# Kernel tuning notes

Measured on AMD Instinct MI355X. Metric: run time of the kernel, lower is better.

The kernel has to match this reference:

```python
import jax, jax.numpy as jnp
import numpy as np

KERNEL = 3
DILATIONS = (2, 3)
NUM_HEADS = 8


def _unfold_windows(t, k, dil):
    # t: [B, C, H, W] -> [B, C, k*k, H, W], same layout as nn.Unfold(k, dil, pad=dil*(k-1)//2)
    B, C, H, W = t.shape
    pad = dil * (k - 1) // 2
    tp = jnp.pad(t, ((0, 0), (0, 0), (pad, pad), (pad, pad)))
    ws = [tp[:, :, i * dil:i * dil + H, j * dil:j * dil + W]
          for i in range(k) for j in range(k)]
    return jnp.stack(ws, axis=2)


def _dilate_attention(q, k_, v, kernel, dil, head_dim):
    # q,k_,v: [B, d, H, W]
    B, d, H, W = q.shape
    nh = d // head_dim
    scale = head_dim ** (-0.5)
    qh = q.reshape(B, nh, head_dim, H, W)
    kw = _unfold_windows(k_, kernel, dil).reshape(B, nh, head_dim, kernel * kernel, H, W)
    vw = _unfold_windows(v, kernel, dil).reshape(B, nh, head_dim, kernel * kernel, H, W)
    attn = jax.nn.softmax(jnp.einsum('bndhw,bndkhw->bnkhw', qh, kw) * scale, axis=2)
    out = jnp.einsum('bnkhw,bndkhw->bndhw', attn, vw)  # [B, nh, hd, H, W]
    return out.transpose(0, 3, 4, 1, 2).reshape(B, H, W, d)


def setup_inputs() -> dict:
    key = jax.random.key(0)
    k1, k2, k3, k4 = jax.random.split(key, 4)
    B, H, W, C = 4, 128, 128, 256
    x = jax.random.normal(k1, (B, H, W, C), dtype=jnp.float32)
    Wqkv = jax.random.normal(k2, (3 * C, C), dtype=jnp.float32) * (C ** -0.5)
    Wproj = jax.random.normal(k3, (C, C), dtype=jnp.float32) * (C ** -0.5)
    bproj = jnp.zeros((C,), dtype=jnp.float32)
    return {"x": x, "Wqkv": Wqkv, "Wproj": Wproj, "bproj": bproj}


def reference(x, Wqkv, Wproj, bproj):
    B, H, W, C = x.shape
    nd = len(DILATIONS)
    head_dim = C // NUM_HEADS
    # 1x1 conv qkv (no bias), then split into 3 and nd dilation groups
    qkv = jnp.einsum('bhwc,oc->bohw', x, Wqkv).reshape(B, 3, nd, C // nd, H, W)
    outs = []
    for i, dil in enumerate(DILATIONS):
        q, k_, v = qkv[:, 0, i], qkv[:, 1, i], qkv[:, 2, i]
        outs.append(_dilate_attention(q, k_, v, KERNEL, dil, head_dim))
    xo = jnp.concatenate(outs, axis=-1)  # [B, H, W, C], dilation-group-major channels
    return jnp.einsum('bhwc,oc->bhwo', xo, Wproj) + bproj
```

## Files before the change

### kernel.cpp

```cpp
#include <hip/hip_runtime.h>
#include <stdint.h>


typedef __attribute__((ext_vector_type(8))) short bf16x8;
typedef __attribute__((ext_vector_type(4))) float f32x4;

__device__ __forceinline__ void unpack2(unsigned u, float& lo, float& hi) {
  union { unsigned u; float f; } a, b;
  a.u = u << 16;
  b.u = u & 0xffff0000u;
  lo = a.f; hi = b.f;
}
__device__ __forceinline__ unsigned short f2bf(float f) {
  union { float f; unsigned u; } x; x.f = f;
  unsigned r = x.u + 0x7fffu + ((x.u >> 16) & 1u);
  return (unsigned short)(r >> 16);
}
__device__ __forceinline__ unsigned pk2bf(float a, float b) {
  return (unsigned)f2bf(a) | ((unsigned)f2bf(b) << 16);
}

__global__ __launch_bounds__(256) void cvt_f32_to_bf16(
    const float* __restrict__ src, unsigned short* __restrict__ dst, int n) {
  int i = (blockIdx.x * 256 + threadIdx.x) * 8;
  if (i + 8 <= n) {
    const float4* s = (const float4*)(src + i);
    float4 a = s[0], b = s[1];
    uint4 o;
    o.x = pk2bf(a.x, a.y); o.y = pk2bf(a.z, a.w);
    o.z = pk2bf(b.x, b.y); o.w = pk2bf(b.z, b.w);
    *(uint4*)(dst + i) = o;
  } else {
    for (; i < n; ++i) dst[i] = f2bf(src[i]);
  }
}

#define BARX()                                                \
  do {                                                        \
    asm volatile("s_waitcnt lgkmcnt(0)" ::: "memory");        \
    __builtin_amdgcn_s_barrier();                             \
    __builtin_amdgcn_sched_barrier(0);                        \
  } while (0)
#define WAITVM(n)                                             \
  do {                                                        \
    asm volatile("s_waitcnt vmcnt(" #n ")" ::: "memory");     \
    __builtin_amdgcn_sched_barrier(0);                        \
  } while (0)

template <int OUTF32>
__global__ __launch_bounds__(256) void gemm_bt(
    const unsigned short* __restrict__ A, const unsigned short* __restrict__ B,
    void* __restrict__ Cout, const float* __restrict__ bias,
    int N, int NT) {
  __shared__ __align__(16) unsigned short lds[4][8192];

  const int tid  = threadIdx.x;
  const int lane = tid & 63;
  const int wv   = tid >> 6;
  const int wr   = wv >> 1;
  const int wc   = wv & 1;

  const int nwg = gridDim.x;
  const int q8  = nwg >> 3;
  const int nid = (blockIdx.x & 7) * q8 + (blockIdx.x >> 3);
  const int n0  = (nid % NT) * 128;
  const int m0  = (nid / NT) * 128;

  const int stg_row = wv * 8 + (lane >> 3);
  const int stg_k   = ((lane & 7) ^ (lane >> 3)) * 8;
  const unsigned short* Ag = A + (size_t)(m0 + stg_row) * 256 + stg_k;
  const unsigned short* Bg = B + (size_t)(n0 + stg_row) * 256 + stg_k;

  f32x4 acc[4][4];
#pragma unroll
  for (int i = 0; i < 4; ++i)
#pragma unroll
    for (int j = 0; j < 4; ++j) acc[i][j] = (f32x4){0.f, 0.f, 0.f, 0.f};

  const int a_r = lane & 15;
  const int rsw = lane & 7;

#define STAGE(buf, kt)                                                         \
  do {                                                                         \
    const unsigned short* Asrc = Ag + (kt) * 64;                               \
    const unsigned short* Bsrc = Bg + (kt) * 64;                               \
    _Pragma("unroll")                                                          \
    for (int it = 0; it < 4; ++it) {                                           \
      __builtin_amdgcn_global_load_lds(                                        \
          (const __attribute__((address_space(1))) void*)(Asrc + (size_t)it * 32 * 256), \
          (__attribute__((address_space(3))) void*)&lds[(buf) * 2][it * 2048 + wv * 512], \
          16, 0, 0);                                                           \
      __builtin_amdgcn_global_load_lds(                                        \
          (const __attribute__((address_space(1))) void*)(Bsrc + (size_t)it * 32 * 256), \
          (__attribute__((address_space(3))) void*)&lds[(buf) * 2 + 1][it * 2048 + wv * 512], \
          16, 0, 0);                                                           \
    }                                                                          \
  } while (0)

#define COMPUTE(buf)                                                           \
  do {                                                                         \
    _Pragma("unroll")                                                          \
    for (int kk = 0; kk < 64; kk += 32) {                                      \
      const int gsw = (((kk >> 3) + (lane >> 4)) ^ rsw) * 8;  \
      bf16x8 af[4], bfr[4];                                                    \
      _Pragma("unroll")                                                        \
      for (int mi = 0; mi < 4; ++mi)                                           \
        af[mi] = *(const bf16x8*)&lds[(buf) * 2][(wr * 64 + mi * 16 + a_r) * 64 + gsw]; \
      _Pragma("unroll")                                                        \
      for (int ni = 0; ni < 4; ++ni)                                           \
        bfr[ni] = *(const bf16x8*)&lds[(buf) * 2 + 1][(wc * 64 + ni * 16 + a_r) * 64 + gsw]; \
      _Pragma("unroll")                                                        \
      for (int mi = 0; mi < 4; ++mi)                                           \
        _Pragma("unroll")                                                      \
        for (int ni = 0; ni < 4; ++ni)                                         \
          acc[mi][ni] = __builtin_amdgcn_mfma_f32_16x16x32_bf16(               \
              af[mi], bfr[ni], acc[mi][ni], 0, 0, 0);                          \
    }                                                                          \
  } while (0)

  STAGE(0, 0);
  STAGE(1, 1);
  WAITVM(8);  BARX();
  COMPUTE(0);
  BARX();
  STAGE(0, 2);
  WAITVM(8);  BARX();
  COMPUTE(1);
  BARX();
  STAGE(1, 3);
  WAITVM(8);  BARX();
  COMPUTE(0);
  BARX();
  WAITVM(0);  BARX();
  COMPUTE(1);
  BARX();

  const int cl = wc * 64 + a_r;
  const int rl = wr * 64 + (lane >> 4) * 4;
  if (!OUTF32) {
    unsigned short* eb = &lds[0][0];
#pragma unroll
    for (int ni = 0; ni < 4; ++ni)
#pragma unroll
      for (int mi = 0; mi < 4; ++mi)
#pragma unroll
        for (int r = 0; r < 4; ++r)
          eb[(rl + mi * 16 + r) * 136 + cl + ni * 16] = f2bf(acc[mi][ni][r]);
    BARX();
    unsigned short* C = (unsigned short*)Cout;
#pragma unroll
    for (int p = 0; p < 8; ++p) {
      const int idx = p * 256 + tid;
      const int row = idx >> 4;
      const int seg = idx & 15;
      uint4 v = *(const uint4*)&eb[row * 136 + seg * 8];
      *(uint4*)&C[(size_t)(m0 + row) * N + n0 + seg * 8] = v;
    }
  } else {
    float* ef = (float*)&lds[0][0];
    float* C = (float*)Cout;
    float bv[4];
#pragma unroll
    for (int ni = 0; ni < 4; ++ni) bv[ni] = bias[n0 + wc * 64 + ni * 16 + a_r];
#pragma unroll
    for (int half = 0; half < 2; ++half) {
      if (wr == half) {
        const int rb = (lane >> 4) * 4;
#pragma unroll
        for (int ni = 0; ni < 4; ++ni)
#pragma unroll
          for (int mi = 0; mi < 4; ++mi)
#pragma unroll
            for (int r = 0; r < 4; ++r)
              ef[(rb + mi * 16 + r) * 132 + wc * 64 + ni * 16 + a_r] =
                  acc[mi][ni][r] + bv[ni];
      }
      BARX();
#pragma unroll
      for (int p = 0; p < 8; ++p) {
        const int idx = p * 256 + tid;
        const int row = idx >> 5;
        const int seg = idx & 31;
        f32x4 v = *(const f32x4*)&ef[row * 132 + seg * 4];
        *(f32x4*)&C[(size_t)(m0 + half * 64 + row) * N + n0 + seg * 4] = v;
      }
      BARX();
    }
  }
#undef STAGE
#undef COMPUTE
}

__global__ __launch_bounds__(256) void attn_kernel(
    const unsigned short* __restrict__ qkv, unsigned short* __restrict__ xo) {
  const int nwg = gridDim.x;
  const int q8  = nwg >> 3;
  const int bid = (blockIdx.x & 7) * q8 + (blockIdx.x >> 3);
  const int gid   = bid * 256 + threadIdx.x;
  const int combo = gid & 7;
  const int pixel = gid >> 3;
  const int w = pixel & 127;
  const int h = (pixel >> 7) & 127;
  const int b = pixel >> 14;
  const int branch = combo >> 2;
  const int dil = branch ? 3 : 2;
  const int choff = combo * 32;

  const unsigned short* qp = qkv + (size_t)pixel * 768 + choff;
  float q[32];
#pragma unroll
  for (int t = 0; t < 4; ++t) {
    uint4 u = *(const uint4*)(qp + t * 8);
    unpack2(u.x, q[t * 8 + 0], q[t * 8 + 1]);
    unpack2(u.y, q[t * 8 + 2], q[t * 8 + 3]);
    unpack2(u.z, q[t * 8 + 4], q[t * 8 + 5]);
    unpack2(u.w, q[t * 8 + 6], q[t * 8 + 7]);
  }

  float sc[9];
#pragma unroll
  for (int i = 0; i < 3; ++i) {
#pragma unroll
    for (int j = 0; j < 3; ++j) {
      const int hh = h + (i - 1) * dil;
      const int ww = w + (j - 1) * dil;
      float s = 0.f;
      if ((unsigned)hh < 128u && (unsigned)ww < 128u) {
        const unsigned short* kp =
            qkv + (size_t)((((b << 7) | hh) << 7) | ww) * 768 + 256 + choff;
#pragma unroll
        for (int t = 0; t < 4; ++t) {
          uint4 u = *(const uint4*)(kp + t * 8);
          float a0, a1;
          unpack2(u.x, a0, a1); s += q[t * 8 + 0] * a0 + q[t * 8 + 1] * a1;
          unpack2(u.y, a0, a1); s += q[t * 8 + 2] * a0 + q[t * 8 + 3] * a1;
          unpack2(u.z, a0, a1); s += q[t * 8 + 4] * a0 + q[t * 8 + 5] * a1;
          unpack2(u.w, a0, a1); s += q[t * 8 + 6] * a0 + q[t * 8 + 7] * a1;
        }
      }
      sc[i * 3 + j] = s * 0.17677669529663687f;
    }
  }

  float mx = sc[0];
#pragma unroll
  for (int t = 1; t < 9; ++t) mx = fmaxf(mx, sc[t]);
  float wgt[9], sum = 0.f;
#pragma unroll
  for (int t = 0; t < 9; ++t) { wgt[t] = __expf(sc[t] - mx); sum += wgt[t]; }
  const float inv = 1.f / sum;

  float o[32];
#pragma unroll
  for (int t = 0; t < 32; ++t) o[t] = 0.f;
#pragma unroll
  for (int i = 0; i < 3; ++i) {
#pragma unroll
    for (int j = 0; j < 3; ++j) {
      const int hh = h + (i - 1) * dil;
      const int ww = w + (j - 1) * dil;
      if ((unsigned)hh < 128u && (unsigned)ww < 128u) {
        const float wv = wgt[i * 3 + j] * inv;
        const unsigned short* vp =
            qkv + (size_t)((((b << 7) | hh) << 7) | ww) * 768 + 512 + choff;
#pragma unroll
        for (int t = 0; t < 4; ++t) {
          uint4 u = *(const uint4*)(vp + t * 8);
          float a0, a1;
          unpack2(u.x, a0, a1); o[t * 8 + 0] += wv * a0; o[t * 8 + 1] += wv * a1;
          unpack2(u.y, a0, a1); o[t * 8 + 2] += wv * a0; o[t * 8 + 3] += wv * a1;
          unpack2(u.z, a0, a1); o[t * 8 + 4] += wv * a0; o[t * 8 + 5] += wv * a1;
          unpack2(u.w, a0, a1); o[t * 8 + 6] += wv * a0; o[t * 8 + 7] += wv * a1;
        }
      }
    }
  }

  unsigned short* op = xo + (size_t)pixel * 256 + choff;
#pragma unroll
  for (int t = 0; t < 4; ++t) {
    uint4 u;
    u.x = pk2bf(o[t * 8 + 0], o[t * 8 + 1]);
    u.y = pk2bf(o[t * 8 + 2], o[t * 8 + 3]);
    u.z = pk2bf(o[t * 8 + 4], o[t * 8 + 5]);
    u.w = pk2bf(o[t * 8 + 6], o[t * 8 + 7]);
    *(uint4*)(op + t * 8) = u;
  }
}

extern "C" void kernel_launch(void* const* d_in, const int* in_sizes, int n_in,
                              void* d_out, int out_size, void* d_ws, size_t ws_size,
                              hipStream_t stream) {
  const float* x     = (const float*)d_in[0];
  const float* Wqkv  = (const float*)d_in[1];
  const float* Wproj = (const float*)d_in[2];
  const float* bproj = (const float*)d_in[3];

  const int M = 4 * 128 * 128;
  const int C = 256;

  unsigned short* xb     = (unsigned short*)d_ws;
  unsigned short* qkvb   = xb + (size_t)M * C;
  unsigned short* xob    = qkvb + (size_t)M * 3 * C;
  unsigned short* wqkvb  = xob + (size_t)M * C;
  unsigned short* wprojb = wqkvb + (size_t)3 * C * C;

  cvt_f32_to_bf16<<<(M * C / 8 + 255) / 256, 256, 0, stream>>>(x, xb, M * C);
  cvt_f32_to_bf16<<<(3 * C * C / 8 + 255) / 256, 256, 0, stream>>>(Wqkv, wqkvb, 3 * C * C);
  cvt_f32_to_bf16<<<(C * C / 8 + 255) / 256, 256, 0, stream>>>(Wproj, wprojb, C * C);

  gemm_bt<0><<<(M / 128) * (3 * C / 128), 256, 0, stream>>>(
      xb, wqkvb, (void*)qkvb, nullptr, 3 * C, 3 * C / 128);

  attn_kernel<<<(M * 8) / 256, 256, 0, stream>>>(qkvb, xob);

  gemm_bt<1><<<(M / 128) * (C / 128), 256, 0, stream>>>(
      xob, wprojb, d_out, bproj, C, C / 128);
}
```

Measured before the change: 136.3 us.

## Split attention head across two lanes with packed f32x2 math and batched loads

Each head-pixel is now handled by two threads, each covering 16 channels, and the partial dot products are combined with a lane shuffle. This doubles thread count and halves per-thread registers, which should raise occupancy and memory-level parallelism. K/V loads for a whole window row are issued up front, using predicated zero values instead of branches. Math uses packed float2 vectors so the compiler can emit packed FMA instructions, and the softmax scale is folded into q. The cost is extra shuffles and a larger grid.

```diff
diff --git a/kernel.cpp b/kernel.cpp
--- a/kernel.cpp
+++ b/kernel.cpp
@@ -4,12 +4,13 @@
 
 typedef __attribute__((ext_vector_type(8))) short bf16x8;
 typedef __attribute__((ext_vector_type(4))) float f32x4;
-
-__device__ __forceinline__ void unpack2(unsigned u, float& lo, float& hi) {
+typedef __attribute__((ext_vector_type(2))) float f32x2;
+
+__device__ __forceinline__ f32x2 up2(unsigned u) {
   union { unsigned u; float f; } a, b;
   a.u = u << 16;
   b.u = u & 0xffff0000u;
-  lo = a.f; hi = b.f;
+  return (f32x2){a.f, b.f};
 }
 __device__ __forceinline__ unsigned short f2bf(float f) {
   union { float f; unsigned u; } x; x.f = f;
@@ -197,95 +198,108 @@
   const int q8  = nwg >> 3;
   const int bid = (blockIdx.x & 7) * q8 + (blockIdx.x >> 3);
   const int gid   = bid * 256 + threadIdx.x;
-  const int combo = gid & 7;
-  const int pixel = gid >> 3;
+  const int half  = gid & 1;
+  const int combo = (gid >> 1) & 7;
+  const int pixel = gid >> 4;
   const int w = pixel & 127;
   const int h = (pixel >> 7) & 127;
   const int b = pixel >> 14;
-  const int branch = combo >> 2;
-  const int dil = branch ? 3 : 2;
-  const int choff = combo * 32;
+  const int dil = (combo >> 2) ? 3 : 2;
+  const int choff = combo * 32 + half * 16;
 
   const unsigned short* qp = qkv + (size_t)pixel * 768 + choff;
-  float q[32];
-#pragma unroll
-  for (int t = 0; t < 4; ++t) {
-    uint4 u = *(const uint4*)(qp + t * 8);
-    unpack2(u.x, q[t * 8 + 0], q[t * 8 + 1]);
-    unpack2(u.y, q[t * 8 + 2], q[t * 8 + 3]);
-    unpack2(u.z, q[t * 8 + 4], q[t * 8 + 5]);
-    unpack2(u.w, q[t * 8 + 6], q[t * 8 + 7]);
-  }
+  f32x2 q2[8];
+  {
+    uint4 u0 = *(const uint4*)qp;
+    uint4 u1 = *(const uint4*)(qp + 8);
+    const f32x2 s2 = {0.17677669529663687f, 0.17677669529663687f};
+    q2[0] = up2(u0.x) * s2; q2[1] = up2(u0.y) * s2;
+    q2[2] = up2(u0.z) * s2; q2[3] = up2(u0.w) * s2;
+    q2[4] = up2(u1.x) * s2; q2[5] = up2(u1.y) * s2;
+    q2[6] = up2(u1.z) * s2; q2[7] = up2(u1.w) * s2;
+  }
+
+  const uint4 z4 = make_uint4(0u, 0u, 0u, 0u);
 
   float sc[9];
 #pragma unroll
   for (int i = 0; i < 3; ++i) {
+    const int hh = h + (i - 1) * dil;
+    const bool vrow = (unsigned)hh < 128u;
+    uint4 ka[3], kb[3];
 #pragma unroll
     for (int j = 0; j < 3; ++j) {
-      const int hh = h + (i - 1) * dil;
       const int ww = w + (j - 1) * dil;
-      float s = 0.f;
-      if ((unsigned)hh < 128u && (unsigned)ww < 128u) {
-        const unsigned short* kp =
-            qkv + (size_t)((((b << 7) | hh) << 7) | ww) * 768 + 256 + choff;
-#pragma unroll
-        for (int t = 0; t < 4; ++t) {
-          uint4 u = *(const uint4*)(kp + t * 8);
-          float a0, a1;
-          unpack2(u.x, a0, a1); s += q[t * 8 + 0] * a0 + q[t * 8 + 1] * a1;
-          unpack2(u.y, a0, a1); s += q[t * 8 + 2] * a0 + q[t * 8 + 3] * a1;
-          unpack2(u.z, a0, a1); s += q[t * 8 + 4] * a0 + q[t * 8 + 5] * a1;
-          unpack2(u.w, a0, a1); s += q[t * 8 + 6] * a0 + q[t * 8 + 7] * a1;
-        }
-      }
-      sc[i * 3 + j] = s * 0.17677669529663687f;
-    }
-  }
+      const bool ok = vrow && ((unsigned)ww < 128u);
+      const unsigned short* kp =
+          qkv + (size_t)((((b << 7) | hh) << 7) | ww) * 768 + 256 + choff;
+      ka[j] = ok ? *(const uint4*)kp : z4;
+      kb[j] = ok ? *(const uint4*)(kp + 8) : z4;
+    }
+#pragma unroll
+    for (int j = 0; j < 3; ++j) {
+      f32x2 a = q2[0] * up2(ka[j].x);
+      a += q2[1] * up2(ka[j].y);
+      a += q2[2] * up2(ka[j].z);
+      a += q2[3] * up2(ka[j].w);
+      a += q2[4] * up2(kb[j].x);
+      a += q2[5] * up2(kb[j].y);
+      a += q2[6] * up2(kb[j].z);
+      a += q2[7] * up2(kb[j].w);
+      sc[i * 3 + j] = a.x + a.y;
+    }
+  }
+#pragma unroll
+  for (int t = 0; t < 9; ++t) sc[t] += __shfl_xor(sc[t], 1);
 
   float mx = sc[0];
 #pragma unroll
   for (int t = 1; t < 9; ++t) mx = fmaxf(mx, sc[t]);
-  float wgt[9], sum = 0.f;
-#pragma unroll
-  for (int t = 0; t < 9; ++t) { wgt[t] = __expf(sc[t] - mx); sum += wgt[t]; }
+  float sum = 0.f;
+#pragma unroll
+  for (int t = 0; t < 9; ++t) { sc[t] = __expf(sc[t] - mx); sum += sc[t]; }
   const float inv = 1.f / sum;
 
-  float o[32];
-#pragma unroll
-  for (int t = 0; t < 32; ++t) o[t] = 0.f;
+  f32x2 o2[8];
+#pragma unroll
+  for (int t = 0; t < 8; ++t) o2[t] = (f32x2){0.f, 0.f};
 #pragma unroll
   for (int i = 0; i < 3; ++i) {
+    const int hh = h + (i - 1) * dil;
+    const bool vrow = (unsigned)hh < 128u;
+    uint4 va[3], vb[3];
 #pragma unroll
     for (int j = 0; j < 3; ++j) {
-      const int hh = h + (i - 1) * dil;
       const int ww = w + (j - 1) * dil;
-      if ((unsigned)hh < 128u && (unsigned)ww < 128u) {
-        const float wv = wgt[i * 3 + j] * inv;
-        const unsigned short* vp =
-            qkv + (size_t)((((b << 7) | hh) << 7) | ww) * 768 + 512 + choff;
-#pragma unroll
-        for (int t = 0; t < 4; ++t) {
-          uint4 u = *(const uint4*)(vp + t * 8);
-          float a0, a1;
-          unpack2(u.x, a0, a1); o[t * 8 + 0] += wv * a0; o[t * 8 + 1] += wv * a1;
-          unpack2(u.y, a0, a1); o[t * 8 + 2] += wv * a0; o[t * 8 + 3] += wv * a1;
-          unpack2(u.z, a0, a1); o[t * 8 + 4] += wv * a0; o[t * 8 + 5] += wv * a1;
-          unpack2(u.w, a0, a1); o[t * 8 + 6] += wv * a0; o[t * 8 + 7] += wv * a1;
-        }
-      }
+      const bool ok = vrow && ((unsigned)ww < 128u);
+      const unsigned short* vp =
+          qkv + (size_t)((((b << 7) | hh) << 7) | ww) * 768 + 512 + choff;
+      va[j] = ok ? *(const uint4*)vp : z4;
+      vb[j] = ok ? *(const uint4*)(vp + 8) : z4;
+    }
+#pragma unroll
+    for (int j = 0; j < 3; ++j) {
+      const float wv = sc[i * 3 + j] * inv;
+      const f32x2 w2 = {wv, wv};
+      o2[0] += w2 * up2(va[j].x);
+      o2[1] += w2 * up2(va[j].y);
+      o2[2] += w2 * up2(va[j].z);
+      o2[3] += w2 * up2(va[j].w);
+      o2[4] += w2 * up2(vb[j].x);
+      o2[5] += w2 * up2(vb[j].y);
+      o2[6] += w2 * up2(vb[j].z);
+      o2[7] += w2 * up2(vb[j].w);
     }
   }
 
   unsigned short* op = xo + (size_t)pixel * 256 + choff;
-#pragma unroll
-  for (int t = 0; t < 4; ++t) {
-    uint4 u;
-    u.x = pk2bf(o[t * 8 + 0], o[t * 8 + 1]);
-    u.y = pk2bf(o[t * 8 + 2], o[t * 8 + 3]);
-    u.z = pk2bf(o[t * 8 + 4], o[t * 8 + 5]);
-    u.w = pk2bf(o[t * 8 + 6], o[t * 8 + 7]);
-    *(uint4*)(op + t * 8) = u;
-  }
+  uint4 s0, s1;
+  s0.x = pk2bf(o2[0].x, o2[0].y); s0.y = pk2bf(o2[1].x, o2[1].y);
+  s0.z = pk2bf(o2[2].x, o2[2].y); s0.w = pk2bf(o2[3].x, o2[3].y);
+  s1.x = pk2bf(o2[4].x, o2[4].y); s1.y = pk2bf(o2[5].x, o2[5].y);
+  s1.z = pk2bf(o2[6].x, o2[6].y); s1.w = pk2bf(o2[7].x, o2[7].y);
+  *(uint4*)op = s0;
+  *(uint4*)(op + 8) = s1;
 }
 
 extern "C" void kernel_launch(void* const* d_in, const int* in_sizes, int n_in,
@@ -312,7 +326,7 @@
   gemm_bt<0><<<(M / 128) * (3 * C / 128), 256, 0, stream>>>(
       xb, wqkvb, (void*)qkvb, nullptr, 3 * C, 3 * C / 128);
 
-  attn_kernel<<<(M * 8) / 256, 256, 0, stream>>>(qkvb, xob);
+  attn_kernel<<<(M * 16) / 256, 256, 0, stream>>>(qkvb, xob);
 
   gemm_bt<1><<<(M / 128) * (C / 128), 256, 0, stream>>>(
       xob, wprojb, d_out, bproj, C, C / 128);
```

Result: slower. 313.5 us (+130.0%).
